# Optimization experiments

Hardware: AMD Instinct MI355X
Metric: run time of the kernel (lower is better)

## Reference

```python
import jax, jax.numpy as jnp
import numpy as np

B, NPTS, T, P, C, D = 2, 32768, 32768, 512, 4, 768


def _sincos_pos_embed(centers, embed_dim):
    # centers: np [P,3]; matches get_3d_sincos_pos_embed
    c = centers - centers.mean(axis=0)
    c = c / np.linalg.norm(c, axis=1).max()
    div = np.exp(np.arange(0, embed_dim, 6) * -(np.log(10000.0) / embed_dim))  # [D/6]
    arg = c[:, None, :] * div[None, :, None]                                   # [P, D/6, 3]
    pe = np.concatenate([np.sin(arg), np.cos(arg)], axis=-1).reshape(centers.shape[0], embed_dim)
    return pe.astype(np.float32)


def setup_inputs() -> dict:
    key = jax.random.key(0)
    ks = jax.random.split(key, 12)
    rng = np.random.default_rng(0)

    # ragged patch sizes (avg 64) summing exactly to T
    sizes = rng.integers(32, 97, size=P).astype(np.int64)
    sizes = np.maximum((sizes * (T / sizes.sum())).astype(np.int64), 1)
    sizes[-1] += T - sizes.sum()
    patch_offset = jnp.asarray(np.concatenate([[0], np.cumsum(sizes)]), dtype=jnp.int32)  # [P+1]

    patch_index = jax.random.randint(ks[0], (T,), 0, NPTS, dtype=jnp.int32)
    latent = jax.random.normal(ks[1], (B, NPTS, C), dtype=jnp.float32)

    s = 0.02
    params = dict(
        w1a=jax.random.normal(ks[2], (C, D), jnp.float32) * s,
        b1a=jnp.zeros((D,), jnp.float32),
        w1b=jax.random.normal(ks[3], (D, D), jnp.float32) * s,
        b1b=jnp.zeros((D,), jnp.float32),
        w2a=jax.random.normal(ks[4], (2 * D, D), jnp.float32) * s,
        b2a=jnp.zeros((D,), jnp.float32),
        g2=jnp.ones((D,), jnp.float32),
        beta2=jnp.zeros((D,), jnp.float32),
        w2b=jax.random.normal(ks[5], (D, D), jnp.float32) * s,
        b2b=jnp.zeros((D,), jnp.float32),
    )

    centers = rng.standard_normal((P, 3))
    pos_embed = jnp.asarray(_sincos_pos_embed(centers, D))[None]  # [1, P, D]

    return dict(latent=latent, patch_index=patch_index, patch_offset=patch_offset,
                pos_embed=pos_embed, **params)


def _ln(x, eps, gamma=None, beta=None):
    mu = x.mean(axis=-1, keepdims=True)
    var = ((x - mu) ** 2).mean(axis=-1, keepdims=True)
    y = (x - mu) * jax.lax.rsqrt(var + eps)
    if gamma is not None:
        y = y * gamma + beta
    return y


def reference(latent, patch_index, patch_offset, pos_embed,
              w1a, b1a, w1b, b1b, w2a, b2a, g2, beta2, w2b, b2b):
    T_ = patch_index.shape[0]
    P_ = patch_offset.shape[0] - 1
    # segment id of each token (repeat_interleave inverse): seg[t] = patch containing t
    seg = jnp.searchsorted(patch_offset[1:], jnp.arange(T_, dtype=patch_offset.dtype), side='right')

    x = latent[:, patch_index, :]                           # [B, T, C] gather
    h = x @ w1a + b1a
    h = jax.nn.gelu(_ln(h, 1e-6), approximate=False)
    h = h @ w1b + b1b                                       # [B, T, D]

    segmax = lambda a: jax.ops.segment_max(a, seg, num_segments=P_)
    y = jax.vmap(segmax)(h)                                 # [B, P, D] ragged max-pool

    h2 = jnp.concatenate([y[:, seg, :], h], axis=-1)        # repeat_interleave + concat
    h2 = h2 @ w2a + b2a
    h2 = jax.nn.gelu(_ln(h2, 1e-5, g2, beta2), approximate=False)
    h2 = h2 @ w2b + b2b                                     # [B, T, D]
    raw_latent = h2

    out = jax.vmap(segmax)(raw_latent) + pos_embed          # [B, P, D]
    return out.astype(raw_latent.dtype), raw_latent
```

## Files before the change

kernel.cpp:

```cpp
#include <hip/hip_runtime.h>
#include <hip/hip_bf16.h>
#include <math.h>

#define B_    2
#define NPTS_ 32768
#define T_    32768
#define P_    512
#define C_    4
#define D_    768
#define M_    (B_ * T_)

typedef __bf16 bf16_t;
typedef __bf16 bf16x8 __attribute__((ext_vector_type(8)));
typedef __bf16 bf16x4 __attribute__((ext_vector_type(4)));
typedef float  f32x4  __attribute__((ext_vector_type(4)));

__device__ inline void gload16(const void* g, void* l) {
  __builtin_amdgcn_global_load_lds(
      (const __attribute__((address_space(1))) void*)g,
      (__attribute__((address_space(3))) void*)l, 16, 0, 0);
}

__device__ inline float gelu_exact(float x) {
  return 0.5f * x * (1.0f + erff(x * 0.70710678118654752f));
}

__device__ inline unsigned fmap(float x) {
  unsigned u = __float_as_uint(x);
  return (u & 0x80000000u) ? ~u : (u | 0x80000000u);
}
__device__ inline float funmap(unsigned u) {
  unsigned v = (u & 0x80000000u) ? (u & 0x7FFFFFFFu) : ~u;
  return __uint_as_float(v);
}

__global__ __launch_bounds__(256) void prep_kernel(
    const int* __restrict__ off, int* __restrict__ seg, uint4* __restrict__ umax,
    const float* __restrict__ w1b, const float* __restrict__ w2a,
    const float* __restrict__ w2b,
    bf16_t* __restrict__ w1bT, bf16_t* __restrict__ w2aTT,
    bf16_t* __restrict__ w2aBT, bf16_t* __restrict__ w2bT) {
  __shared__ float tile[32][33];
  int bid = blockIdx.x, tid = threadIdx.x;
  if (bid < 2304) {
    const float* src; bf16_t* dst;
    int which = bid / 576, r = bid - which * 576;
    if (which == 0)      { src = w1b;             dst = w1bT;  }
    else if (which == 1) { src = w2a;             dst = w2aTT; }
    else if (which == 2) { src = w2a + D_ * D_;   dst = w2aBT; }
    else                 { src = w2b;             dst = w2bT;  }
    int n0 = (r % 24) * 32, k0 = (r / 24) * 32;
    int tx = tid & 31, ty = tid >> 5;
    #pragma unroll
    for (int i = 0; i < 4; ++i)
      tile[ty + 8 * i][tx] = src[(size_t)(k0 + ty + 8 * i) * D_ + n0 + tx];
    __syncthreads();
    #pragma unroll
    for (int i = 0; i < 4; ++i)
      dst[(size_t)(n0 + ty + 8 * i) * D_ + k0 + tx] = (bf16_t)tile[tx][ty + 8 * i];
  } else if (bid < 2432) {
    int t = (bid - 2304) * 256 + tid;
    int lo = 0, hi = P_;
    while (lo < hi) {
      int mid = (lo + hi) >> 1;
      if (off[mid + 1] <= t) lo = mid + 1; else hi = mid;
    }
    seg[t] = lo;
  } else {
    umax[(size_t)(bid - 2432) * 256 + tid] = make_uint4(0, 0, 0, 0);
  }
}

__global__ __launch_bounds__(256) void yconv_kernel(
    const uint4* __restrict__ ymax, bf16_t* __restrict__ y) {
  int t = blockIdx.x * 256 + threadIdx.x;
  uint4 u = ymax[t];
  bf16x4 o;
  o[0] = (bf16_t)funmap(u.x); o[1] = (bf16_t)funmap(u.y);
  o[2] = (bf16_t)funmap(u.z); o[3] = (bf16_t)funmap(u.w);
  *(bf16x4*)(y + (size_t)t * 4) = o;
}

__global__ __launch_bounds__(256) void final2_kernel(
    const uint4* __restrict__ rmax, const float4* __restrict__ pe,
    float4* __restrict__ out) {
  int t = blockIdx.x * 256 + threadIdx.x;
  int row = t / 192, col = t % 192;
  uint4 u = rmax[t];
  float4 p = pe[(row & (P_ - 1)) * 192 + col];
  float4 o;
  o.x = funmap(u.x) + p.x; o.y = funmap(u.y) + p.y;
  o.z = funmap(u.z) + p.z; o.w = funmap(u.w) + p.w;
  out[t] = o;
}

__global__ __launch_bounds__(256) void embed_kernel(
    const float4* __restrict__ latent4, const int* __restrict__ pidx,
    const float* __restrict__ w1a, const float* __restrict__ b1a,
    bf16_t* __restrict__ act1) {
  int wid = threadIdx.x >> 6, lane = threadIdx.x & 63;
  int m = blockIdx.x * 4 + wid;
  int b = m >> 15, t = m & (T_ - 1);
  float4 x = latent4[(size_t)b * NPTS_ + pidx[t]];
  int d8 = lane * 8, d4 = 512 + lane * 4;
  float v[12];
  {
    float4 a0 = *(const float4*)(b1a + d8);
    float4 a1 = *(const float4*)(b1a + d8 + 4);
    float4 a2 = *(const float4*)(b1a + d4);
    v[0]=a0.x; v[1]=a0.y; v[2]=a0.z; v[3]=a0.w;
    v[4]=a1.x; v[5]=a1.y; v[6]=a1.z; v[7]=a1.w;
    v[8]=a2.x; v[9]=a2.y; v[10]=a2.z; v[11]=a2.w;
  }
  float xk[4] = {x.x, x.y, x.z, x.w};
  #pragma unroll
  for (int k = 0; k < 4; ++k) {
    const float* w = w1a + k * D_;
    float4 w0 = *(const float4*)(w + d8);
    float4 w1 = *(const float4*)(w + d8 + 4);
    float4 w2 = *(const float4*)(w + d4);
    float f = xk[k];
    v[0] += f*w0.x; v[1] += f*w0.y; v[2] += f*w0.z; v[3] += f*w0.w;
    v[4] += f*w1.x; v[5] += f*w1.y; v[6] += f*w1.z; v[7] += f*w1.w;
    v[8] += f*w2.x; v[9] += f*w2.y; v[10]+= f*w2.z; v[11]+= f*w2.w;
  }
  float sum = 0.f, sq = 0.f;
  #pragma unroll
  for (int j = 0; j < 12; ++j) { sum += v[j]; sq += v[j]*v[j]; }
  #pragma unroll
  for (int o = 32; o > 0; o >>= 1) { sum += __shfl_xor(sum, o); sq += __shfl_xor(sq, o); }
  float mu = sum * (1.0f / D_);
  float rstd = rsqrtf(sq * (1.0f / D_) - mu * mu + 1e-6f);
  bf16x8 o8; bf16x4 o4;
  #pragma unroll
  for (int j = 0; j < 8; ++j) o8[j] = (bf16_t)gelu_exact((v[j] - mu) * rstd);
  #pragma unroll
  for (int j = 0; j < 4; ++j) o4[j] = (bf16_t)gelu_exact((v[8 + j] - mu) * rstd);
  size_t base = (size_t)m * D_;
  *(bf16x8*)(act1 + base + d8) = o8;
  *(bf16x4*)(act1 + base + d4) = o4;
}

__global__ __launch_bounds__(256) void ln2_kernel(
    const bf16_t* __restrict__ h2pre, const float* __restrict__ z,
    const int* __restrict__ seg, const float* __restrict__ g2,
    const float* __restrict__ beta2, bf16_t* __restrict__ act2) {
  int wid = threadIdx.x >> 6, lane = threadIdx.x & 63;
  int m = blockIdx.x * 4 + wid;
  int b = m >> 15, t = m & (T_ - 1);
  int d8 = lane * 8, d4 = 512 + lane * 4;
  size_t base = (size_t)m * D_;
  const float* zrow = z + (size_t)((b << 9) + seg[t]) * D_;
  bf16x8 i8 = *(const bf16x8*)(h2pre + base + d8);
  bf16x4 i4 = *(const bf16x4*)(h2pre + base + d4);
  float4 z0 = *(const float4*)(zrow + d8);
  float4 z1 = *(const float4*)(zrow + d8 + 4);
  float4 z2 = *(const float4*)(zrow + d4);
  float v[12];
  #pragma unroll
  for (int j = 0; j < 8; ++j) v[j] = (float)i8[j];
  #pragma unroll
  for (int j = 0; j < 4; ++j) v[8 + j] = (float)i4[j];
  v[0]+=z0.x; v[1]+=z0.y; v[2]+=z0.z; v[3]+=z0.w;
  v[4]+=z1.x; v[5]+=z1.y; v[6]+=z1.z; v[7]+=z1.w;
  v[8]+=z2.x; v[9]+=z2.y; v[10]+=z2.z; v[11]+=z2.w;
  float sum = 0.f, sq = 0.f;
  #pragma unroll
  for (int j = 0; j < 12; ++j) { sum += v[j]; sq += v[j]*v[j]; }
  #pragma unroll
  for (int o = 32; o > 0; o >>= 1) { sum += __shfl_xor(sum, o); sq += __shfl_xor(sq, o); }
  float mu = sum * (1.0f / D_);
  float rstd = rsqrtf(sq * (1.0f / D_) - mu * mu + 1e-5f);
  float4 ga = *(const float4*)(g2 + d8);
  float4 gb = *(const float4*)(g2 + d8 + 4);
  float4 gc = *(const float4*)(g2 + d4);
  float4 ba = *(const float4*)(beta2 + d8);
  float4 bb = *(const float4*)(beta2 + d8 + 4);
  float4 bc = *(const float4*)(beta2 + d4);
  float g[12] = {ga.x,ga.y,ga.z,ga.w, gb.x,gb.y,gb.z,gb.w, gc.x,gc.y,gc.z,gc.w};
  float be[12]= {ba.x,ba.y,ba.z,ba.w, bb.x,bb.y,bb.z,bb.w, bc.x,bc.y,bc.z,bc.w};
  bf16x8 o8; bf16x4 o4;
  #pragma unroll
  for (int j = 0; j < 8; ++j) o8[j] = (bf16_t)gelu_exact((v[j] - mu) * rstd * g[j] + be[j]);
  #pragma unroll
  for (int j = 0; j < 4; ++j) o4[j] = (bf16_t)gelu_exact((v[8+j] - mu) * rstd * g[8+j] + be[8+j]);
  *(bf16x8*)(act2 + base + d8) = o8;
  *(bf16x4*)(act2 + base + d4) = o4;
}

#define STAGE_A(P2, KTG)                                                     \
  { _Pragma("unroll")                                                        \
    for (int h = 0; h < 2; ++h) {                                            \
      _Pragma("unroll")                                                      \
      for (int ps = 0; ps < 2; ++ps) {                                       \
        int c = ps * 512 + wid * 64 + lane;                                  \
        int rw = c >> 3;                                                     \
        int cs = (c & 7) ^ (rw & 7);                                         \
        gload16(A + (size_t)(m0 + h * 128 + rw) * 768 + (KTG) + cs * 8,      \
                lds + (P2) * 65536 + h * 16384 + ps * 8192 + wid * 1024);    \
      } } }

#define STAGE_B(P2, KTG)                                                     \
  { _Pragma("unroll")                                                        \
    for (int h = 0; h < 2; ++h) {                                            \
      _Pragma("unroll")                                                      \
      for (int ps = 0; ps < 2; ++ps) {                                       \
        int c = ps * 512 + wid * 64 + lane;                                  \
        int rw = c >> 3;                                                     \
        int cs = (c & 7) ^ (rw & 7);                                         \
        gload16(BT + (size_t)(n0 + h * 128 + rw) * 768 + (KTG) + cs * 8,     \
                lds + (P2) * 65536 + 32768 + h * 16384 + ps * 8192 + wid * 1024); \
      } } }

#define READ_AF0(BASE)                                                       \
  { _Pragma("unroll")                                                        \
    for (int i = 0; i < 4; ++i) {                                            \
      _Pragma("unroll")                                                      \
      for (int s = 0; s < 2; ++s) {                                          \
        int row = i * 16 + lr;                                               \
        int ch = (s * 4 + hi) ^ cx;                                          \
        af0[i][s] = *(const bf16x8*)((BASE) + wm * 16384 + row * 128 + ch * 16); \
      } } }

#define READ_BF0(BASE)                                                       \
  { _Pragma("unroll")                                                        \
    for (int jb = 0; jb < 2; ++jb) {                                         \
      _Pragma("unroll")                                                      \
      for (int s = 0; s < 2; ++s) {                                          \
        int nrow = wn * 64 + jb * 16 + lr;                                   \
        int ch = (s * 4 + hi) ^ cx;                                          \
        bf0[jb][s] = *(const bf16x8*)((BASE) + 32768 + (nrow >> 7) * 16384 + \
                                      (nrow & 127) * 128 + ch * 16);         \
      } } }

template <bool HASBIAS, bool SEGMAX, typename OutT>
__global__ __launch_bounds__(512, 1) void gemm256_kernel(
    const bf16_t* __restrict__ A, const bf16_t* __restrict__ BT,
    const float* __restrict__ bias, OutT* __restrict__ C,
    const int* __restrict__ seg, unsigned* __restrict__ gmax) {
  constexpr int NT = 12;
  __shared__ __align__(16) char lds[131072];
  __shared__ int segm[256];
  int tid = threadIdx.x;
  int wid = tid >> 6, lane = tid & 63;
  int lr = lane & 15, hi = lane >> 4;
  int wm = wid >> 2, wn = wid & 3;

  int gx = gridDim.x;
  int nb = gx * gridDim.y;
  int bid = blockIdx.y * gx + blockIdx.x;
  int w = ((nb & 7) == 0) ? ((bid & 7) * (nb >> 3) + (bid >> 3)) : bid;
  int bx = w % gx, by = w / gx;
  int n0 = bx * 256, m0 = by * 256;

  if (SEGMAX) { if (tid < 256) segm[tid] = seg[(m0 + tid) & (T_ - 1)]; }

  f32x4 acc[8][4] = {};
  bf16x8 af0[4][2], af1[4][2], bf0[2][2], bf1[2][2];
  int cx = lr & 7;

  STAGE_A(0, 0); STAGE_B(0, 0);
  STAGE_A(1, 64); STAGE_B(1, 64);
  asm volatile("s_waitcnt vmcnt(8)" ::: "memory");
  __builtin_amdgcn_s_barrier();
  READ_AF0(lds); READ_BF0(lds);

  for (int j = 0; j < NT; ++j) {
    const char* base  = lds + (j & 1) * 65536;
    const char* baseN = lds + ((j & 1) ^ 1) * 65536;

    #pragma unroll
    for (int i = 0; i < 4; ++i)
      #pragma unroll
      for (int s = 0; s < 2; ++s) {
        int row = 64 + i * 16 + lr;
        int ch = (s * 4 + hi) ^ cx;
        af1[i][s] = *(const bf16x8*)(base + wm * 16384 + row * 128 + ch * 16);
      }
    __builtin_amdgcn_s_setprio(1);
    #pragma unroll
    for (int i = 0; i < 4; ++i)
      #pragma unroll
      for (int jb = 0; jb < 2; ++jb)
        #pragma unroll
        for (int s = 0; s < 2; ++s)
          acc[i][jb] = __builtin_amdgcn_mfma_f32_16x16x32_bf16(bf0[jb][s], af0[i][s], acc[i][jb], 0, 0, 0);
    __builtin_amdgcn_s_setprio(0);
    __builtin_amdgcn_s_barrier();

    #pragma unroll
    for (int jb = 0; jb < 2; ++jb)
      #pragma unroll
      for (int s = 0; s < 2; ++s) {
        int nrow = wn * 64 + 32 + jb * 16 + lr;
        int ch = (s * 4 + hi) ^ cx;
        bf1[jb][s] = *(const bf16x8*)(base + 32768 + (nrow >> 7) * 16384 +
                                      (nrow & 127) * 128 + ch * 16);
      }
    __builtin_amdgcn_s_setprio(1);
    #pragma unroll
    for (int i = 0; i < 4; ++i)
      #pragma unroll
      for (int jb = 0; jb < 2; ++jb)
        #pragma unroll
        for (int s = 0; s < 2; ++s)
          acc[4 + i][jb] = __builtin_amdgcn_mfma_f32_16x16x32_bf16(bf0[jb][s], af1[i][s], acc[4 + i][jb], 0, 0, 0);
    __builtin_amdgcn_s_setprio(0);
    __builtin_amdgcn_s_barrier();

    if (j + 2 < NT) STAGE_A(j & 1, (j + 2) * 64);
    __builtin_amdgcn_s_setprio(1);
    #pragma unroll
    for (int i = 0; i < 4; ++i)
      #pragma unroll
      for (int jb = 0; jb < 2; ++jb)
        #pragma unroll
        for (int s = 0; s < 2; ++s)
          acc[i][2 + jb] = __builtin_amdgcn_mfma_f32_16x16x32_bf16(bf1[jb][s], af0[i][s], acc[i][2 + jb], 0, 0, 0);
    __builtin_amdgcn_s_setprio(0);

    if (j + 1 < NT) {
      if (j + 2 < NT) asm volatile("s_waitcnt vmcnt(4)" ::: "memory");
      else            asm volatile("s_waitcnt vmcnt(0)" ::: "memory");
      __builtin_amdgcn_s_barrier();
      READ_AF0(baseN); READ_BF0(baseN);
      if (j + 2 < NT) STAGE_B(j & 1, (j + 2) * 64);
    }
    __builtin_amdgcn_s_setprio(1);
    #pragma unroll
    for (int i = 0; i < 4; ++i)
      #pragma unroll
      for (int jb = 0; jb < 2; ++jb)
        #pragma unroll
        for (int s = 0; s < 2; ++s)
          acc[4 + i][2 + jb] = __builtin_amdgcn_mfma_f32_16x16x32_bf16(bf1[jb][s], af1[i][s], acc[4 + i][2 + jb], 0, 0, 0);
    __builtin_amdgcn_s_setprio(0);
    __builtin_amdgcn_s_barrier();
  }

  unsigned* smax = reinterpret_cast<unsigned*>(lds);
  int sb = 0, zb = 0;
  if (SEGMAX) {
    sb = segm[0];
    zb = (m0 >> 15) << 9;
    for (int q = tid; q < 16 * 256; q += 512) smax[q] = 0u;
    __syncthreads();
  }

  f32x4 bvv[4];
  #pragma unroll
  for (int jb = 0; jb < 4; ++jb) {
    if (HASBIAS) {
      const float* bp = bias + n0 + wn * 64 + jb * 16 + hi * 4;
      bvv[jb][0] = bp[0]; bvv[jb][1] = bp[1]; bvv[jb][2] = bp[2]; bvv[jb][3] = bp[3];
    } else {
      bvv[jb][0] = bvv[jb][1] = bvv[jb][2] = bvv[jb][3] = 0.f;
    }
  }

  #pragma unroll
  for (int i = 0; i < 8; ++i) {
    size_t ro = (size_t)(m0 + wm * 128 + i * 16 + lr) * 768 + (n0 + wn * 64 + hi * 4);
    #pragma unroll
    for (int jb = 0; jb < 4; ++jb) {
      f32x4 v = acc[i][jb] + bvv[jb];
      if constexpr (sizeof(OutT) == 4) {
        *reinterpret_cast<f32x4*>(C + ro + jb * 16) = v;
      } else {
        bf16x4 o;
        #pragma unroll
        for (int r = 0; r < 4; ++r) o[r] = (bf16_t)v[r];
        *reinterpret_cast<bf16x4*>(C + ro + jb * 16) = o;
      }
    }
  }

  if (SEGMAX) {
    int lrow = wm * 128 + lr;
    #pragma unroll
    for (int jb = 0; jb < 4; ++jb) {
      int nl = wn * 64 + jb * 16 + hi * 4;
      f32x4 run = acc[0][jb] + bvv[jb];
      int ps = segm[lrow];
      #pragma unroll
      for (int i = 1; i < 8; ++i) {
        int cs2 = segm[lrow + i * 16];
        f32x4 v = acc[i][jb] + bvv[jb];
        if (cs2 != ps) {
          #pragma unroll
          for (int r = 0; r < 4; ++r)
            atomicMax(&smax[(ps - sb) * 256 + nl + r], fmap(run[r]));
          run = v; ps = cs2;
        } else {
          #pragma unroll
          for (int r = 0; r < 4; ++r) run[r] = fmaxf(run[r], v[r]);
        }
      }
      #pragma unroll
      for (int r = 0; r < 4; ++r)
        atomicMax(&smax[(ps - sb) * 256 + nl + r], fmap(run[r]));
    }
    __syncthreads();
    int nseg = segm[255] - sb + 1;
    int mlo = m0 & (T_ - 1);
    bool strad_lo = (mlo != 0) && (seg[(mlo - 1)] == sb);
    bool strad_hi = (mlo + 256 < T_) && (seg[(mlo + 256)] == segm[255]);
    for (int q = tid; q < nseg * 256; q += 512) {
      int sl = q >> 8, nl2 = q & 255;
      unsigned val = smax[q];
      unsigned* dst = &gmax[(size_t)(zb + sb + sl) * 768 + n0 + nl2];
      bool bdry = (sl == 0 && strad_lo) || (sl == nseg - 1 && strad_hi);
      if (bdry) atomicMax(dst, val);
      else      *dst = val;
    }
  }
}

extern "C" void kernel_launch(void* const* d_in, const int* in_sizes, int n_in,
                              void* d_out, int out_size, void* d_ws, size_t ws_size,
                              hipStream_t stream) {
  const float* latent       = (const float*)d_in[0];
  const int*   patch_index  = (const int*)d_in[1];
  const int*   patch_offset = (const int*)d_in[2];
  const float* pos_embed    = (const float*)d_in[3];
  const float* w1a  = (const float*)d_in[4];
  const float* b1a  = (const float*)d_in[5];
  const float* w1b  = (const float*)d_in[6];
  const float* b1b  = (const float*)d_in[7];
  const float* w2a  = (const float*)d_in[8];
  const float* b2a  = (const float*)d_in[9];
  const float* g2   = (const float*)d_in[10];
  const float* beta2= (const float*)d_in[11];
  const float* w2b  = (const float*)d_in[12];
  const float* b2b  = (const float*)d_in[13];

  float* out_f   = (float*)d_out;
  float* raw_out = out_f + (size_t)B_ * P_ * D_;

  char* ws = (char*)d_ws;
  size_t off = 0;
  auto take = [&](size_t bytes) {
    off = (off + 255) & ~(size_t)255;
    char* p = ws + off;
    off += bytes;
    return p;
  };
  int*      seg   = (int*)     take((size_t)T_ * 4);
  bf16_t*   w1bT  = (bf16_t*)  take((size_t)D_ * D_ * 2);
  bf16_t*   w2aTT = (bf16_t*)  take((size_t)D_ * D_ * 2);
  bf16_t*   w2aBT = (bf16_t*)  take((size_t)D_ * D_ * 2);
  bf16_t*   w2bT  = (bf16_t*)  take((size_t)D_ * D_ * 2);
  bf16_t*   ybuf  = (bf16_t*)  take((size_t)B_ * P_ * D_ * 2);
  float*    zbuf  = (float*)   take((size_t)B_ * P_ * D_ * 4);
  unsigned* umax  = (unsigned*)take((size_t)2 * B_ * P_ * D_ * 4);
  unsigned* ymax  = umax;
  unsigned* rmax  = umax + (size_t)B_ * P_ * D_;
  bf16_t*   bufY  = (bf16_t*)  take((size_t)M_ * D_ * 2);
  size_t needX = (size_t)M_ * D_ * 2;
  size_t offX  = (off + 255) & ~(size_t)255;
  bf16_t* bufX;
  if (offX + needX <= ws_size) {
    bufX = (bf16_t*)take(needX);
  } else {
    bufX = (bf16_t*)raw_out;
  }

  prep_kernel<<<3968, 256, 0, stream>>>(patch_offset, seg, (uint4*)umax,
                                        w1b, w2a, w2b, w1bT, w2aTT, w2aBT, w2bT);

  embed_kernel<<<M_ / 4, 256, 0, stream>>>((const float4*)latent, patch_index, w1a, b1a, bufX);

  gemm256_kernel<true, true, bf16_t><<<dim3(3, M_/256), 512, 0, stream>>>(
      bufX, w1bT, b1b, bufY, seg, ymax);

  yconv_kernel<<<(B_ * P_ * D_) / (4 * 256), 256, 0, stream>>>((const uint4*)ymax, ybuf);

  gemm256_kernel<true, false, float><<<dim3(3, (B_*P_)/256), 512, 0, stream>>>(
      ybuf, w2aTT, b2a, zbuf, nullptr, nullptr);

  gemm256_kernel<false, false, bf16_t><<<dim3(3, M_/256), 512, 0, stream>>>(
      bufY, w2aBT, nullptr, bufX, nullptr, nullptr);

  ln2_kernel<<<M_ / 4, 256, 0, stream>>>(bufX, zbuf, seg, g2, beta2, bufY);

  gemm256_kernel<true, true, float><<<dim3(3, M_/256), 512, 0, stream>>>(
      bufY, w2bT, b2b, raw_out, seg, rmax);

  final2_kernel<<<(B_ * P_ * D_) / (4 * 256), 256, 0, stream>>>(
      (const uint4*)rmax, (const float4*)pos_embed, (float4*)out_f);
}
```

Before: 440.3 us.

## Fold w1b into w2a bottom half and fuse first GEMM with h-side projection

Precomputes the product of w1b and the bottom half of w2a, plus the combined bias, so the first big GEMM produces both h (for segment max) and the h-part of the second layer in one N=1536 pass. This removes the separate M×768×768 GEMM that read h back from memory. The embed step is merged into the prep kernel, and ln2 now works in place. The trade-offs are an extra small GEMM and bias kernel, a wider first GEMM, and extra bf16 rounding from the pre-multiplied weights.

```diff
diff --git a/kernel.cpp b/kernel.cpp
--- a/kernel.cpp
+++ b/kernel.cpp
@@ -34,18 +34,74 @@
   return __uint_as_float(v);
 }
 
-__global__ __launch_bounds__(256) void prep_kernel(
+__global__ __launch_bounds__(256) void bigprep_kernel(
+    const float4* __restrict__ latent4, const int* __restrict__ pidx,
+    const float* __restrict__ w1a, const float* __restrict__ b1a,
+    bf16_t* __restrict__ act1,
     const int* __restrict__ off, int* __restrict__ seg, uint4* __restrict__ umax,
     const float* __restrict__ w1b, const float* __restrict__ w2a,
-    const float* __restrict__ w2b,
-    bf16_t* __restrict__ w1bT, bf16_t* __restrict__ w2aTT,
-    bf16_t* __restrict__ w2aBT, bf16_t* __restrict__ w2bT) {
-  __shared__ float tile[32][33];
+    const float* __restrict__ w2b, const float* __restrict__ b1b,
+    bf16_t* __restrict__ wBig, bf16_t* __restrict__ w2aTT,
+    bf16_t* __restrict__ w2aBT, bf16_t* __restrict__ w2bT,
+    bf16_t* __restrict__ w1bR, float* __restrict__ bBig) {
   int bid = blockIdx.x, tid = threadIdx.x;
-  if (bid < 2304) {
+  if (bid < 4096) {
+    int wid = tid >> 6, lane = tid & 63;
+    int mb = bid * 16 + wid * 4;
+    int d8 = lane * 8, d4 = 512 + lane * 4;
+    float bb[12], wreg[4][12];
+    {
+      float4 a0 = *(const float4*)(b1a + d8);
+      float4 a1 = *(const float4*)(b1a + d8 + 4);
+      float4 a2 = *(const float4*)(b1a + d4);
+      bb[0]=a0.x; bb[1]=a0.y; bb[2]=a0.z; bb[3]=a0.w;
+      bb[4]=a1.x; bb[5]=a1.y; bb[6]=a1.z; bb[7]=a1.w;
+      bb[8]=a2.x; bb[9]=a2.y; bb[10]=a2.z; bb[11]=a2.w;
+    }
+    #pragma unroll
+    for (int k = 0; k < 4; ++k) {
+      const float* w = w1a + k * D_;
+      float4 w0 = *(const float4*)(w + d8);
+      float4 w1 = *(const float4*)(w + d8 + 4);
+      float4 w2 = *(const float4*)(w + d4);
+      wreg[k][0]=w0.x; wreg[k][1]=w0.y; wreg[k][2]=w0.z; wreg[k][3]=w0.w;
+      wreg[k][4]=w1.x; wreg[k][5]=w1.y; wreg[k][6]=w1.z; wreg[k][7]=w1.w;
+      wreg[k][8]=w2.x; wreg[k][9]=w2.y; wreg[k][10]=w2.z; wreg[k][11]=w2.w;
+    }
+    for (int rr = 0; rr < 4; ++rr) {
+      int m = mb + rr;
+      int b = m >> 15, t = m & (T_ - 1);
+      float4 x = latent4[(size_t)b * NPTS_ + pidx[t]];
+      float xk[4] = {x.x, x.y, x.z, x.w};
+      float v[12];
+      #pragma unroll
+      for (int j = 0; j < 12; ++j) {
+        v[j] = bb[j];
+        #pragma unroll
+        for (int k = 0; k < 4; ++k) v[j] += xk[k] * wreg[k][j];
+      }
+      float sum = 0.f, sq = 0.f;
+      #pragma unroll
+      for (int j = 0; j < 12; ++j) { sum += v[j]; sq += v[j]*v[j]; }
+      #pragma unroll
+      for (int o = 32; o > 0; o >>= 1) { sum += __shfl_xor(sum, o); sq += __shfl_xor(sq, o); }
+      float mu = sum * (1.0f / D_);
+      float rstd = rsqrtf(sq * (1.0f / D_) - mu * mu + 1e-6f);
+      bf16x8 o8; bf16x4 o4;
+      #pragma unroll
+      for (int j = 0; j < 8; ++j) o8[j] = (bf16_t)gelu_exact((v[j] - mu) * rstd);
+      #pragma unroll
+      for (int j = 0; j < 4; ++j) o4[j] = (bf16_t)gelu_exact((v[8 + j] - mu) * rstd);
+      size_t base = (size_t)m * D_;
+      *(bf16x8*)(act1 + base + d8) = o8;
+      *(bf16x4*)(act1 + base + d4) = o4;
+    }
+  } else if (bid < 6400) {
+    __shared__ float tile[32][33];
+    int r = bid - 4096;
     const float* src; bf16_t* dst;
-    int which = bid / 576, r = bid - which * 576;
-    if (which == 0)      { src = w1b;             dst = w1bT;  }
+    int which = r / 576; r -= which * 576;
+    if (which == 0)      { src = w1b;             dst = wBig;  }
     else if (which == 1) { src = w2a;             dst = w2aTT; }
     else if (which == 2) { src = w2a + D_ * D_;   dst = w2aBT; }
     else                 { src = w2b;             dst = w2bT;  }
@@ -58,8 +114,19 @@
     #pragma unroll
     for (int i = 0; i < 4; ++i)
       dst[(size_t)(n0 + ty + 8 * i) * D_ + k0 + tx] = (bf16_t)tile[tx][ty + 8 * i];
-  } else if (bid < 2432) {
-    int t = (bid - 2304) * 256 + tid;
+  } else if (bid < 6688) {
+    size_t i8 = ((size_t)(bid - 6400) * 256 + tid) * 8;
+    float4 a = *(const float4*)(w1b + i8);
+    float4 b = *(const float4*)(w1b + i8 + 4);
+    bf16x8 o;
+    o[0]=(bf16_t)a.x; o[1]=(bf16_t)a.y; o[2]=(bf16_t)a.z; o[3]=(bf16_t)a.w;
+    o[4]=(bf16_t)b.x; o[5]=(bf16_t)b.y; o[6]=(bf16_t)b.z; o[7]=(bf16_t)b.w;
+    *(bf16x8*)(w1bR + i8) = o;
+  } else if (bid < 6691) {
+    int n = (bid - 6688) * 256 + tid;
+    bBig[n] = b1b[n];
+  } else if (bid < 6819) {
+    int t = (bid - 6691) * 256 + tid;
     int lo = 0, hi = P_;
     while (lo < hi) {
       int mid = (lo + hi) >> 1;
@@ -67,8 +134,68 @@
     }
     seg[t] = lo;
   } else {
-    umax[(size_t)(bid - 2432) * 256 + tid] = make_uint4(0, 0, 0, 0);
-  }
+    umax[(size_t)(bid - 6819) * 256 + tid] = make_uint4(0, 0, 0, 0);
+  }
+}
+
+__global__ __launch_bounds__(256) void bcombo_kernel(
+    const float* __restrict__ b1b, const bf16_t* __restrict__ WcT,
+    float* __restrict__ bc) {
+  int n = blockIdx.x * 256 + threadIdx.x;
+  float s = 0.f;
+  for (int k = 0; k < D_; k += 8) {
+    bf16x8 w = *(const bf16x8*)(WcT + (size_t)n * D_ + k);
+    #pragma unroll
+    for (int j = 0; j < 8; ++j) s += b1b[k + j] * (float)w[j];
+  }
+  bc[n] = s;
+}
+
+__global__ __launch_bounds__(256) void ln2_kernel(
+    bf16_t* __restrict__ h2, const float* __restrict__ z,
+    const int* __restrict__ seg, const float* __restrict__ g2,
+    const float* __restrict__ beta2) {
+  int wid = threadIdx.x >> 6, lane = threadIdx.x & 63;
+  int m = blockIdx.x * 4 + wid;
+  int b = m >> 15, t = m & (T_ - 1);
+  int d8 = lane * 8, d4 = 512 + lane * 4;
+  size_t base = (size_t)m * D_;
+  const float* zrow = z + (size_t)((b << 9) + seg[t]) * D_;
+  bf16x8 i8 = *(const bf16x8*)(h2 + base + d8);
+  bf16x4 i4 = *(const bf16x4*)(h2 + base + d4);
+  float4 z0 = *(const float4*)(zrow + d8);
+  float4 z1 = *(const float4*)(zrow + d8 + 4);
+  float4 z2 = *(const float4*)(zrow + d4);
+  float v[12];
+  #pragma unroll
+  for (int j = 0; j < 8; ++j) v[j] = (float)i8[j];
+  #pragma unroll
+  for (int j = 0; j < 4; ++j) v[8 + j] = (float)i4[j];
+  v[0]+=z0.x; v[1]+=z0.y; v[2]+=z0.z; v[3]+=z0.w;
+  v[4]+=z1.x; v[5]+=z1.y; v[6]+=z1.z; v[7]+=z1.w;
+  v[8]+=z2.x; v[9]+=z2.y; v[10]+=z2.z; v[11]+=z2.w;
+  float sum = 0.f, sq = 0.f;
+  #pragma unroll
+  for (int j = 0; j < 12; ++j) { sum += v[j]; sq += v[j]*v[j]; }
+  #pragma unroll
+  for (int o = 32; o > 0; o >>= 1) { sum += __shfl_xor(sum, o); sq += __shfl_xor(sq, o); }
+  float mu = sum * (1.0f / D_);
+  float rstd = rsqrtf(sq * (1.0f / D_) - mu * mu + 1e-5f);
+  float4 ga = *(const float4*)(g2 + d8);
+  float4 gb = *(const float4*)(g2 + d8 + 4);
+  float4 gc = *(const float4*)(g2 + d4);
+  float4 ba = *(const float4*)(beta2 + d8);
+  float4 bbv = *(const float4*)(beta2 + d8 + 4);
+  float4 bc = *(const float4*)(beta2 + d4);
+  float g[12] = {ga.x,ga.y,ga.z,ga.w, gb.x,gb.y,gb.z,gb.w, gc.x,gc.y,gc.z,gc.w};
+  float be[12]= {ba.x,ba.y,ba.z,ba.w, bbv.x,bbv.y,bbv.z,bbv.w, bc.x,bc.y,bc.z,bc.w};
+  bf16x8 o8; bf16x4 o4;
+  #pragma unroll
+  for (int j = 0; j < 8; ++j) o8[j] = (bf16_t)gelu_exact((v[j] - mu) * rstd * g[j] + be[j]);
+  #pragma unroll
+  for (int j = 0; j < 4; ++j) o4[j] = (bf16_t)gelu_exact((v[8+j] - mu) * rstd * g[8+j] + be[8+j]);
+  *(bf16x8*)(h2 + base + d8) = o8;
+  *(bf16x4*)(h2 + base + d4) = o4;
 }
 
 __global__ __launch_bounds__(256) void yconv_kernel(
@@ -94,100 +221,6 @@
   out[t] = o;
 }
 
-__global__ __launch_bounds__(256) void embed_kernel(
-    const float4* __restrict__ latent4, const int* __restrict__ pidx,
-    const float* __restrict__ w1a, const float* __restrict__ b1a,
-    bf16_t* __restrict__ act1) {
-  int wid = threadIdx.x >> 6, lane = threadIdx.x & 63;
-  int m = blockIdx.x * 4 + wid;
-  int b = m >> 15, t = m & (T_ - 1);
-  float4 x = latent4[(size_t)b * NPTS_ + pidx[t]];
-  int d8 = lane * 8, d4 = 512 + lane * 4;
-  float v[12];
-  {
-    float4 a0 = *(const float4*)(b1a + d8);
-    float4 a1 = *(const float4*)(b1a + d8 + 4);
-    float4 a2 = *(const float4*)(b1a + d4);
-    v[0]=a0.x; v[1]=a0.y; v[2]=a0.z; v[3]=a0.w;
-    v[4]=a1.x; v[5]=a1.y; v[6]=a1.z; v[7]=a1.w;
-    v[8]=a2.x; v[9]=a2.y; v[10]=a2.z; v[11]=a2.w;
-  }
-  float xk[4] = {x.x, x.y, x.z, x.w};
-  #pragma unroll
-  for (int k = 0; k < 4; ++k) {
-    const float* w = w1a + k * D_;
-    float4 w0 = *(const float4*)(w + d8);
-    float4 w1 = *(const float4*)(w + d8 + 4);
-    float4 w2 = *(const float4*)(w + d4);
-    float f = xk[k];
-    v[0] += f*w0.x; v[1] += f*w0.y; v[2] += f*w0.z; v[3] += f*w0.w;
-    v[4] += f*w1.x; v[5] += f*w1.y; v[6] += f*w1.z; v[7] += f*w1.w;
-    v[8] += f*w2.x; v[9] += f*w2.y; v[10]+= f*w2.z; v[11]+= f*w2.w;
-  }
-  float sum = 0.f, sq = 0.f;
-  #pragma unroll
-  for (int j = 0; j < 12; ++j) { sum += v[j]; sq += v[j]*v[j]; }
-  #pragma unroll
-  for (int o = 32; o > 0; o >>= 1) { sum += __shfl_xor(sum, o); sq += __shfl_xor(sq, o); }
-  float mu = sum * (1.0f / D_);
-  float rstd = rsqrtf(sq * (1.0f / D_) - mu * mu + 1e-6f);
-  bf16x8 o8; bf16x4 o4;
-  #pragma unroll
-  for (int j = 0; j < 8; ++j) o8[j] = (bf16_t)gelu_exact((v[j] - mu) * rstd);
-  #pragma unroll
-  for (int j = 0; j < 4; ++j) o4[j] = (bf16_t)gelu_exact((v[8 + j] - mu) * rstd);
-  size_t base = (size_t)m * D_;
-  *(bf16x8*)(act1 + base + d8) = o8;
-  *(bf16x4*)(act1 + base + d4) = o4;
-}
-
-__global__ __launch_bounds__(256) void ln2_kernel(
-    const bf16_t* __restrict__ h2pre, const float* __restrict__ z,
-    const int* __restrict__ seg, const float* __restrict__ g2,
-    const float* __restrict__ beta2, bf16_t* __restrict__ act2) {
-  int wid = threadIdx.x >> 6, lane = threadIdx.x & 63;
-  int m = blockIdx.x * 4 + wid;
-  int b = m >> 15, t = m & (T_ - 1);
-  int d8 = lane * 8, d4 = 512 + lane * 4;
-  size_t base = (size_t)m * D_;
-  const float* zrow = z + (size_t)((b << 9) + seg[t]) * D_;
-  bf16x8 i8 = *(const bf16x8*)(h2pre + base + d8);
-  bf16x4 i4 = *(const bf16x4*)(h2pre + base + d4);
-  float4 z0 = *(const float4*)(zrow + d8);
-  float4 z1 = *(const float4*)(zrow + d8 + 4);
-  float4 z2 = *(const float4*)(zrow + d4);
-  float v[12];
-  #pragma unroll
-  for (int j = 0; j < 8; ++j) v[j] = (float)i8[j];
-  #pragma unroll
-  for (int j = 0; j < 4; ++j) v[8 + j] = (float)i4[j];
-  v[0]+=z0.x; v[1]+=z0.y; v[2]+=z0.z; v[3]+=z0.w;
-  v[4]+=z1.x; v[5]+=z1.y; v[6]+=z1.z; v[7]+=z1.w;
-  v[8]+=z2.x; v[9]+=z2.y; v[10]+=z2.z; v[11]+=z2.w;
-  float sum = 0.f, sq = 0.f;
-  #pragma unroll
-  for (int j = 0; j < 12; ++j) { sum += v[j]; sq += v[j]*v[j]; }
-  #pragma unroll
-  for (int o = 32; o > 0; o >>= 1) { sum += __shfl_xor(sum, o); sq += __shfl_xor(sq, o); }
-  float mu = sum * (1.0f / D_);
-  float rstd = rsqrtf(sq * (1.0f / D_) - mu * mu + 1e-5f);
-  float4 ga = *(const float4*)(g2 + d8);
-  float4 gb = *(const float4*)(g2 + d8 + 4);
-  float4 gc = *(const float4*)(g2 + d4);
-  float4 ba = *(const float4*)(beta2 + d8);
-  float4 bb = *(const float4*)(beta2 + d8 + 4);
-  float4 bc = *(const float4*)(beta2 + d4);
-  float g[12] = {ga.x,ga.y,ga.z,ga.w, gb.x,gb.y,gb.z,gb.w, gc.x,gc.y,gc.z,gc.w};
-  float be[12]= {ba.x,ba.y,ba.z,ba.w, bb.x,bb.y,bb.z,bb.w, bc.x,bc.y,bc.z,bc.w};
-  bf16x8 o8; bf16x4 o4;
-  #pragma unroll
-  for (int j = 0; j < 8; ++j) o8[j] = (bf16_t)gelu_exact((v[j] - mu) * rstd * g[j] + be[j]);
-  #pragma unroll
-  for (int j = 0; j < 4; ++j) o4[j] = (bf16_t)gelu_exact((v[8+j] - mu) * rstd * g[8+j] + be[8+j]);
-  *(bf16x8*)(act2 + base + d8) = o8;
-  *(bf16x4*)(act2 + base + d4) = o4;
-}
-
 #define STAGE_A(P2, KTG)                                                     \
   { _Pragma("unroll")                                                        \
     for (int h = 0; h < 2; ++h) {                                            \
@@ -233,7 +266,7 @@
                                       (nrow & 127) * 128 + ch * 16);         \
       } } }
 
-template <bool HASBIAS, bool SEGMAX, typename OutT>
+template <int MODE, bool HASBIAS, typename OutT>
 __global__ __launch_bounds__(512, 1) void gemm256_kernel(
     const bf16_t* __restrict__ A, const bf16_t* __restrict__ BT,
     const float* __restrict__ bias, OutT* __restrict__ C,
@@ -253,7 +286,7 @@
   int bx = w % gx, by = w / gx;
   int n0 = bx * 256, m0 = by * 256;
 
-  if (SEGMAX) { if (tid < 256) segm[tid] = seg[(m0 + tid) & (T_ - 1)]; }
+  if (MODE != 0) { if (tid < 256) segm[tid] = seg[(m0 + tid) & (T_ - 1)]; }
 
   f32x4 acc[8][4] = {};
   bf16x8 af0[4][2], af1[4][2], bf0[2][2], bf1[2][2];
@@ -338,15 +371,6 @@
     __builtin_amdgcn_s_barrier();
   }
 
-  unsigned* smax = reinterpret_cast<unsigned*>(lds);
-  int sb = 0, zb = 0;
-  if (SEGMAX) {
-    sb = segm[0];
-    zb = (m0 >> 15) << 9;
-    for (int q = tid; q < 16 * 256; q += 512) smax[q] = 0u;
-    __syncthreads();
-  }
-
   f32x4 bvv[4];
   #pragma unroll
   for (int jb = 0; jb < 4; ++jb) {
@@ -358,24 +382,35 @@
     }
   }
 
-  #pragma unroll
-  for (int i = 0; i < 8; ++i) {
-    size_t ro = (size_t)(m0 + wm * 128 + i * 16 + lr) * 768 + (n0 + wn * 64 + hi * 4);
-    #pragma unroll
-    for (int jb = 0; jb < 4; ++jb) {
-      f32x4 v = acc[i][jb] + bvv[jb];
-      if constexpr (sizeof(OutT) == 4) {
-        *reinterpret_cast<f32x4*>(C + ro + jb * 16) = v;
-      } else {
-        bf16x4 o;
-        #pragma unroll
-        for (int r = 0; r < 4; ++r) o[r] = (bf16_t)v[r];
-        *reinterpret_cast<bf16x4*>(C + ro + jb * 16) = o;
+  bool is_h = (MODE == 2) && (bx < 3);
+  if (!is_h) {
+    int nc0 = (MODE == 2) ? n0 - 768 : n0;
+    #pragma unroll
+    for (int i = 0; i < 8; ++i) {
+      size_t ro = (size_t)(m0 + wm * 128 + i * 16 + lr) * 768 + (nc0 + wn * 64 + hi * 4);
+      #pragma unroll
+      for (int jb = 0; jb < 4; ++jb) {
+        f32x4 v = acc[i][jb] + bvv[jb];
+        if constexpr (sizeof(OutT) == 4) {
+          *reinterpret_cast<f32x4*>(C + ro + jb * 16) = v;
+        } else {
+          bf16x4 o;
+          #pragma unroll
+          for (int r = 0; r < 4; ++r) o[r] = (bf16_t)v[r];
+          *reinterpret_cast<bf16x4*>(C + ro + jb * 16) = o;
+        }
       }
     }
   }
 
-  if (SEGMAX) {
+  if (MODE == 1 || is_h) {
+    unsigned* smax = reinterpret_cast<unsigned*>(lds);
+    __builtin_amdgcn_s_barrier();
+    int sb = segm[0];
+    int zb = (m0 >> 15) << 9;
+    for (int q = tid; q < 16 * 256; q += 512) smax[q] = 0u;
+    __syncthreads();
+
     int lrow = wm * 128 + lr;
     #pragma unroll
     for (int jb = 0; jb < 4; ++jb) {
@@ -401,10 +436,11 @@
         atomicMax(&smax[(ps - sb) * 256 + nl + r], fmap(run[r]));
     }
     __syncthreads();
+
     int nseg = segm[255] - sb + 1;
     int mlo = m0 & (T_ - 1);
-    bool strad_lo = (mlo != 0) && (seg[(mlo - 1)] == sb);
-    bool strad_hi = (mlo + 256 < T_) && (seg[(mlo + 256)] == segm[255]);
+    bool strad_lo = (mlo != 0) && (seg[mlo - 1] == sb);
+    bool strad_hi = (mlo + 256 < T_) && (seg[mlo + 256] == segm[255]);
     for (int q = tid; q < nseg * 256; q += 512) {
       int sl = q >> 8, nl2 = q & 255;
       unsigned val = smax[q];
@@ -446,10 +482,12 @@
     return p;
   };
   int*      seg   = (int*)     take((size_t)T_ * 4);
-  bf16_t*   w1bT  = (bf16_t*)  take((size_t)D_ * D_ * 2);
+  bf16_t*   wBig  = (bf16_t*)  take((size_t)2 * D_ * D_ * 2);
   bf16_t*   w2aTT = (bf16_t*)  take((size_t)D_ * D_ * 2);
   bf16_t*   w2aBT = (bf16_t*)  take((size_t)D_ * D_ * 2);
   bf16_t*   w2bT  = (bf16_t*)  take((size_t)D_ * D_ * 2);
+  bf16_t*   w1bR  = (bf16_t*)  take((size_t)D_ * D_ * 2);
+  float*    bBig  = (float*)   take((size_t)2 * D_ * 4);
   bf16_t*   ybuf  = (bf16_t*)  take((size_t)B_ * P_ * D_ * 2);
   float*    zbuf  = (float*)   take((size_t)B_ * P_ * D_ * 4);
   unsigned* umax  = (unsigned*)take((size_t)2 * B_ * P_ * D_ * 4);
@@ -465,27 +503,31 @@
     bufX = (bf16_t*)raw_out;
   }
 
-  prep_kernel<<<3968, 256, 0, stream>>>(patch_offset, seg, (uint4*)umax,
-                                        w1b, w2a, w2b, w1bT, w2aTT, w2aBT, w2bT);
-
-  embed_kernel<<<M_ / 4, 256, 0, stream>>>((const float4*)latent, patch_index, w1a, b1a, bufX);
-
-  gemm256_kernel<true, true, bf16_t><<<dim3(3, M_/256), 512, 0, stream>>>(
-      bufX, w1bT, b1b, bufY, seg, ymax);
-
-  yconv_kernel<<<(B_ * P_ * D_) / (4 * 256), 256, 0, stream>>>((const uint4*)ymax, ybuf);
-
-  gemm256_kernel<true, false, float><<<dim3(3, (B_*P_)/256), 512, 0, stream>>>(
+  bigprep_kernel<<<8355, 256, 0, stream>>>(
+      (const float4*)latent, patch_index, w1a, b1a, bufX,
+      patch_offset, seg, (uint4*)umax,
+      w1b, w2a, w2b, b1b,
+      wBig, w2aTT, w2aBT, w2bT, w1bR, bBig);
+
+  gemm256_kernel<0, false, bf16_t><<<dim3(3, 3), 512, 0, stream>>>(
+      w2aBT, w1bR, nullptr, wBig + (size_t)D_ * D_, nullptr, nullptr);
+
+  bcombo_kernel<<<3, 256, 0, stream>>>(b1b, wBig + (size_t)D_ * D_, bBig + D_);
+
+  gemm256_kernel<2, true, bf16_t><<<dim3(6, M_/256), 512, 0, stream>>>(
+      bufX, wBig, bBig, bufY, seg, ymax);
+
+  yconv_kernel<<<(B_ * P_ * D_) / (4 * 256), 256, 0, stream>>>(
+      (const uint4*)ymax, ybuf);
+
+  gemm256_kernel<0, true, float><<<dim3(3, (B_*P_)/256), 512, 0, stream>>>(
       ybuf, w2aTT, b2a, zbuf, nullptr, nullptr);
 
-  gemm256_kernel<false, false, bf16_t><<<dim3(3, M_/256), 512, 0, stream>>>(
-      bufY, w2aBT, nullptr, bufX, nullptr, nullptr);
-
-  ln2_kernel<<<M_ / 4, 256, 0, stream>>>(bufX, zbuf, seg, g2, beta2, bufY);
-
-  gemm256_kernel<true, true, float><<<dim3(3, M_/256), 512, 0, stream>>>(
+  ln2_kernel<<<M_ / 4, 256, 0, stream>>>(bufY, zbuf, seg, g2, beta2);
+
+  gemm256_kernel<1, true, float><<<dim3(3, M_/256), 512, 0, stream>>>(
       bufY, w2bT, b2b, raw_out, seg, rmax);
 
-  final2_kernel<<<(B_ * P_ * D_) / (4 * 256), 256, 0, stream>>>(
+  final2_kernel<<<768, 256, 0, stream>>>(
       (const uint4*)rmax, (const float4*)pos_embed, (float4*)out_f);
 }
```

Result: slower. 498.8 us (+13.3%).
